# Kernel optimization log

Hardware: AMD Instinct MI355X
Metric: run time of the kernel (lower is better)

## Reference

```python
import jax, jax.numpy as jnp
import numpy as np

B, N, C, H = 256, 197, 768, 12
D = C // H  # 64
GRID = 14   # h = w = int(N**0.5); N-1 == 14*14


def setup_inputs() -> dict:
    key = jax.random.key(0)
    ks = jax.random.split(key, 5)
    s = 0.02
    return {
        "x": jax.random.normal(ks[0], (B, N, C), dtype=jnp.float32),
        "W_qkv": jax.random.normal(ks[1], (C, 3 * C), dtype=jnp.float32) * s,
        "b_qkv": jnp.zeros((3 * C,), dtype=jnp.float32),
        "W_proj": jax.random.normal(ks[2], (C, C), dtype=jnp.float32) * s,
        "b_proj": jnp.zeros((C,), dtype=jnp.float32),
        "dwc_w": jax.random.normal(ks[3], (C, 1, 3, 3), dtype=jnp.float32) * s,
        "dwc_b": jnp.zeros((C,), dtype=jnp.float32),
    }


def reference(x, W_qkv, b_qkv, W_proj, b_proj, dwc_w, dwc_b):
    Bx, Nx, Cx = x.shape
    Dh = Cx // H
    h = w = GRID
    # qkv projection -> (3, B, H, N, D)
    qkv = (x @ W_qkv + b_qkv).reshape(Bx, Nx, 3, H, Dh).transpose(2, 0, 3, 1, 4)
    q, k, v = qkv[0], qkv[1], qkv[2]
    scale = Dh ** -0.5
    # graph-candidate attention (softmax candidate): (B, H, N, N)
    attn = jax.nn.softmax(jnp.einsum('bhnd,bhmd->bhnm', q, k) * scale, axis=-1)
    out = jnp.einsum('bhnm,bhmd->bhnd', attn, v)
    out = out.transpose(0, 2, 1, 3).reshape(Bx, Nx, Cx)
    # depthwise conv on V (excluding cls token), residual add into rows 1:
    v_ = v[:, :, 1:, :].transpose(0, 2, 1, 3).reshape(Bx, h, w, Cx).transpose(0, 3, 1, 2)  # (B,C,h,w)
    conv = jax.lax.conv_general_dilated(
        v_, dwc_w, window_strides=(1, 1), padding='SAME',
        feature_group_count=Cx,
        dimension_numbers=('NCHW', 'OIHW', 'NCHW'),
    ) + dwc_b[None, :, None, None]
    out = out.at[:, 1:, :].add(conv.transpose(0, 2, 3, 1).reshape(Bx, Nx - 1, Cx))
    return out @ W_proj + b_proj
```

## Files before the change

kernel.cpp:

```cpp
#include <hip/hip_runtime.h>
#include <hip/hip_bf16.h>

typedef __attribute__((ext_vector_type(8))) short s16x8;
typedef __attribute__((ext_vector_type(4))) float f32x4;

#define MFMA(a, b, c) __builtin_amdgcn_mfma_f32_16x16x32_bf16((a), (b), (c), 0, 0, 0)

__device__ __forceinline__ short f2bf(float f) {
  unsigned u = __builtin_bit_cast(unsigned, f);
  u += 0x7FFFu + ((u >> 16) & 1u);
  return (short)(u >> 16);
}
__device__ __forceinline__ float bf2f(short s) {
  unsigned u = ((unsigned)(unsigned short)s) << 16;
  return __builtin_bit_cast(float, u);
}
__device__ __forceinline__ void async16(const void* g, void* l) {
  __builtin_amdgcn_global_load_lds((const __attribute__((address_space(1))) void*)g,
                                   (__attribute__((address_space(3))) void*)l, 16, 0, 0);
}


__global__ __launch_bounds__(256) void f32_to_bf16_k(const float* __restrict__ in,
                                                     short* __restrict__ out, int n4) {
  int i = blockIdx.x * 256 + threadIdx.x;
  if (i >= n4) return;
  float4 v = ((const float4*)in)[i];
  short4 o;
  o.x = f2bf(v.x); o.y = f2bf(v.y); o.z = f2bf(v.z); o.w = f2bf(v.w);
  ((short4*)out)[i] = o;
}

__global__ __launch_bounds__(256) void transpose_bf16_k(const float* __restrict__ in,
                                                        short* __restrict__ out, int K, int N) {
  int idx = blockIdx.x * 256 + threadIdx.x;
  if (idx >= K * N) return;
  int n = idx / K;
  int k = idx - n * K;
  out[idx] = f2bf(in[k * N + n]);
}

__global__ __launch_bounds__(256) void transpose_dwc_k(const float* __restrict__ in,
                                                       float* __restrict__ out) {
  int idx = blockIdx.x * 256 + threadIdx.x;
  if (idx >= 9 * 768) return;
  int c = idx % 768;
  int tap = idx / 768;
  out[idx] = in[c * 9 + tap];
}


__device__ __forceinline__ void gemm_core(const short* __restrict__ A, const short* __restrict__ Bt,
                                          short* Asm, short* Bsm, int m0, int n0,
                                          f32x4 (&acc)[4][4]) {
  const int tid = threadIdx.x;
  const int lane = tid & 63;
  const int w = tid >> 6;
  const int wm = w >> 1, wn = w & 1;
  const int l15 = lane & 15, qd = lane >> 4;

  for (int kt = 0; kt < 12; ++kt) {
    __syncthreads();
#pragma unroll
    for (int i = 0; i < 4; ++i) {
      int s = i * 256 + tid;
      int row = s >> 3, cst = s & 7;
      int cg = cst ^ (row & 7);
      async16(A + (m0 + row) * 768 + kt * 64 + cg * 8, Asm + s * 8);
      async16(Bt + (n0 + row) * 768 + kt * 64 + cg * 8, Bsm + s * 8);
    }
    __builtin_amdgcn_s_waitcnt(0x0f70);
    __syncthreads();
#pragma unroll
    for (int ks = 0; ks < 2; ++ks) {
      s16x8 af[4], bfr[4];
#pragma unroll
      for (int mt = 0; mt < 4; ++mt) {
        int row = wm * 64 + mt * 16 + l15;
        int kc = ks * 4 + qd;
        af[mt] = *(const s16x8*)(Asm + row * 64 + ((kc ^ (row & 7)) << 3));
      }
#pragma unroll
      for (int nt = 0; nt < 4; ++nt) {
        int row = wn * 64 + nt * 16 + l15;
        int kc = ks * 4 + qd;
        bfr[nt] = *(const s16x8*)(Bsm + row * 64 + ((kc ^ (row & 7)) << 3));
      }
#pragma unroll
      for (int mt = 0; mt < 4; ++mt)
#pragma unroll
        for (int nt = 0; nt < 4; ++nt)
          acc[mt][nt] = MFMA(af[mt], bfr[nt], acc[mt][nt]);
    }
  }
}

__device__ __forceinline__ int xcd_remap(int orig, int nwg) {
  int xcd = orig & 7;
  int grp = orig >> 3;
  int q = nwg >> 3, r = nwg & 7;
  return (xcd < r ? xcd * (q + 1) : r * (q + 1) + (xcd - r) * q) + grp;
}

__global__ __launch_bounds__(256) void gemm_qkv(const short* __restrict__ A, const short* __restrict__ Bt,
                                                const float* __restrict__ bias,
                                                short* __restrict__ qo, short* __restrict__ ko,
                                                short* __restrict__ vo) {
  __shared__ short Asm[128 * 64];
  __shared__ short Bsm[128 * 64];
  const int nwg = 394 * 18;
  int wgid = xcd_remap(blockIdx.x, nwg);
  int mt0 = wgid / 18;
  int nt0 = wgid - mt0 * 18;
  const int m0 = mt0 * 128;
  const int n0 = nt0 * 128;
  const f32x4 z4 = {0.f, 0.f, 0.f, 0.f};
  f32x4 acc[4][4];
#pragma unroll
  for (int i = 0; i < 4; ++i)
#pragma unroll
    for (int j = 0; j < 4; ++j) acc[i][j] = z4;
  gemm_core(A, Bt, Asm, Bsm, m0, n0, acc);

  const int tid = threadIdx.x, lane = tid & 63, w = tid >> 6;
  const int wm = w >> 1, wn = w & 1, l15 = lane & 15, qd = lane >> 4;

  float bv[4];
  short* dstp[4];
  int coff[4];
#pragma unroll
  for (int nt = 0; nt < 4; ++nt) {
    int n = n0 + wn * 64 + nt * 16 + l15;
    bv[nt] = bias[n];
    int s = n / 768;
    int rem = n - s * 768;
    int hh = rem >> 6, d = rem & 63;
    dstp[nt] = (s == 0) ? qo : ((s == 1) ? ko : vo);
    coff[nt] = hh * 197 * 64 + d;
  }
#pragma unroll
  for (int mt = 0; mt < 4; ++mt) {
#pragma unroll
    for (int r = 0; r < 4; ++r) {
      int m = m0 + wm * 64 + mt * 16 + qd * 4 + r;
      int bb = m / 197;
      int tok = m - bb * 197;
      size_t base = (size_t)bb * (12 * 197 * 64) + (size_t)tok * 64;
#pragma unroll
      for (int nt = 0; nt < 4; ++nt)
        dstp[nt][base + coff[nt]] = f2bf(acc[mt][nt][r] + bv[nt]);
    }
  }
}

__global__ __launch_bounds__(256) void gemm_proj(const short* __restrict__ A, const short* __restrict__ Bt,
                                                 const float* __restrict__ bias,
                                                 float* __restrict__ out) {
  __shared__ short Asm[128 * 64];
  __shared__ short Bsm[128 * 64];
  const int nwg = 394 * 6;
  int wgid = xcd_remap(blockIdx.x, nwg);
  int mt0 = wgid / 6;
  int nt0 = wgid - mt0 * 6;
  const int m0 = mt0 * 128;
  const int n0 = nt0 * 128;
  const f32x4 z4 = {0.f, 0.f, 0.f, 0.f};
  f32x4 acc[4][4];
#pragma unroll
  for (int i = 0; i < 4; ++i)
#pragma unroll
    for (int j = 0; j < 4; ++j) acc[i][j] = z4;
  gemm_core(A, Bt, Asm, Bsm, m0, n0, acc);

  const int tid = threadIdx.x, lane = tid & 63, w = tid >> 6;
  const int wm = w >> 1, wn = w & 1, l15 = lane & 15, qd = lane >> 4;
#pragma unroll
  for (int mt = 0; mt < 4; ++mt) {
#pragma unroll
    for (int r = 0; r < 4; ++r) {
      int m = m0 + wm * 64 + mt * 16 + qd * 4 + r;
      float* orow = out + (size_t)m * 768;
#pragma unroll
      for (int nt = 0; nt < 4; ++nt) {
        int n = n0 + wn * 64 + nt * 16 + l15;
        orow[n] = acc[mt][nt][r] + bias[n];
      }
    }
  }
}

__global__ __launch_bounds__(256) void attn_fused(const short* __restrict__ qa, const short* __restrict__ ka,
                                                  const short* __restrict__ va,
                                                  short* __restrict__ aout) {
  __shared__ short Klds[197 * 64];
  __shared__ short Vt[64 * 256];
  __shared__ short Plds[4][16 * 40];

  const int tid = threadIdx.x;
  const int lane = tid & 63;
  const int w = tid >> 6;
  const int l15 = lane & 15, qd = lane >> 4;
  const int bh = blockIdx.x;
  const int b = bh / 12;
  const int h = bh - b * 12;
  const short* kb = ka + (size_t)bh * (197 * 64);
  const short* vb = va + (size_t)bh * (197 * 64);
  const short* qb = qa + (size_t)bh * (197 * 64);

  for (int c = tid; c < 197 * 8; c += 256) {
    int row = c >> 3, cc = c & 7;
    s16x8 v8 = *(const s16x8*)(kb + row * 64 + cc * 8);
    *(s16x8*)(Klds + row * 64 + ((cc ^ (row & 7)) << 3)) = v8;
  }
  for (int c = tid; c < 197 * 8; c += 256) {
    int key = c >> 3, cc = c & 7;
    s16x8 v8 = *(const s16x8*)(vb + key * 64 + cc * 8);
    int kc = key >> 3, km = key & 7;
#pragma unroll
    for (int j = 0; j < 8; ++j) {
      int d = cc * 8 + j;
      Vt[d * 256 + ((kc ^ (d & 7)) << 3) + km] = v8[j];
    }
  }
  for (int i = tid; i < 64 * 27; i += 256) {
    int d = i / 27;
    int key = 197 + (i - d * 27);
    Vt[d * 256 + (((key >> 3) ^ (d & 7)) << 3) + (key & 7)] = 0;
  }
  __syncthreads();

  for (int qt = w; qt < 13; qt += 4) {
    const int m0 = qt * 16;
    int mrow = m0 + l15; if (mrow > 196) mrow = 196;
    s16x8 qf0 = *(const s16x8*)(qb + mrow * 64 + qd * 8);
    s16x8 qf1 = *(const s16x8*)(qb + mrow * 64 + 32 + qd * 8);

    f32x4 S[13];
#pragma unroll
    for (int kt = 0; kt < 13; ++kt) {
      int krow = kt * 16 + l15; if (krow > 196) krow = 196;
      s16x8 kf0 = *(const s16x8*)(Klds + krow * 64 + ((qd ^ (krow & 7)) << 3));
      s16x8 kf1 = *(const s16x8*)(Klds + krow * 64 + (((4 + qd) ^ (krow & 7)) << 3));
      f32x4 sa = {0.f, 0.f, 0.f, 0.f};
      sa = MFMA(qf0, kf0, sa);
      sa = MFMA(qf1, kf1, sa);
      S[kt] = sa;
    }
    const bool maskme = (l15 > 4);
#pragma unroll
    for (int kt = 0; kt < 13; ++kt) {
#pragma unroll
      for (int r = 0; r < 4; ++r) {
        float sv = S[kt][r] * 0.125f;
        if (kt == 12 && maskme) sv = -1e30f;
        S[kt][r] = sv;
      }
    }
    float li[4];
#pragma unroll
    for (int r = 0; r < 4; ++r) {
      float m = S[0][r];
#pragma unroll
      for (int kt = 1; kt < 13; ++kt) m = fmaxf(m, S[kt][r]);
#pragma unroll
      for (int off = 1; off < 16; off <<= 1) m = fmaxf(m, __shfl_xor(m, off));
      float l = 0.f;
#pragma unroll
      for (int kt = 0; kt < 13; ++kt) {
        float p = __builtin_amdgcn_exp2f((S[kt][r] - m) * 1.44269504f);
        S[kt][r] = p;
        l += p;
      }
#pragma unroll
      for (int off = 1; off < 16; off <<= 1) l += __shfl_xor(l, off);
      li[r] = l;
    }

    const f32x4 z4 = {0.f, 0.f, 0.f, 0.f};
    f32x4 O[4] = {z4, z4, z4, z4};
    short* Pw = &Plds[w][0];
#pragma unroll
    for (int kt2 = 0; kt2 < 7; ++kt2) {
#pragma unroll
      for (int sub = 0; sub < 2; ++sub) {
        const int ktile = kt2 * 2 + sub;
#pragma unroll
        for (int r = 0; r < 4; ++r) {
          short pv = 0;
          if (ktile < 13) pv = f2bf(S[ktile][r]);
          Pw[(qd * 4 + r) * 40 + sub * 16 + l15] = pv;
        }
      }
      __builtin_amdgcn_s_waitcnt(0xc07f);
      s16x8 pf = *(const s16x8*)(Pw + l15 * 40 + qd * 8);
#pragma unroll
      for (int nt = 0; nt < 4; ++nt) {
        int d = nt * 16 + l15;
        s16x8 vf = *(const s16x8*)(Vt + d * 256 + (((kt2 * 4 + qd) ^ (d & 7)) << 3));
        O[nt] = MFMA(pf, vf, O[nt]);
      }
    }

#pragma unroll
    for (int r = 0; r < 4; ++r) {
      int tok = m0 + qd * 4 + r;
      if (tok > 196) continue;
      float linv = __builtin_amdgcn_rcpf(li[r]);
      size_t ob = ((size_t)b * 197 + tok) * 768 + h * 64;
#pragma unroll
      for (int nt = 0; nt < 4; ++nt) {
        int d = nt * 16 + l15;
        aout[ob + d] = f2bf(O[nt][r] * linv);
      }
    }
  }
}

__global__ __launch_bounds__(256) void dwconv_add_k(const short* __restrict__ va,
                                                    const float* __restrict__ wT,
                                                    const float* __restrict__ dwcb,
                                                    short* __restrict__ aout) {
  int idx = blockIdx.x * 256 + threadIdx.x;
  if (idx >= 256 * 196 * 96) return;
  int ch = idx % 96;
  int rest = idx / 96;
  int p = rest % 196;
  int b = rest / 196;
  int y = p / 14, x = p - y * 14;
  int c0 = ch * 8;
  int h = c0 >> 6, d0 = c0 & 63;
  const short* vrow = va + (size_t)(b * 12 + h) * (197 * 64) + d0;

  float acc[8];
  float4 b0 = *(const float4*)(dwcb + c0);
  float4 b1 = *(const float4*)(dwcb + c0 + 4);
  acc[0] = b0.x; acc[1] = b0.y; acc[2] = b0.z; acc[3] = b0.w;
  acc[4] = b1.x; acc[5] = b1.y; acc[6] = b1.z; acc[7] = b1.w;

#pragma unroll
  for (int dy = -1; dy <= 1; ++dy) {
    int yy = y + dy;
    if (yy < 0 || yy > 13) continue;
#pragma unroll
    for (int dx = -1; dx <= 1; ++dx) {
      int xx = x + dx;
      if (xx < 0 || xx > 13) continue;
      int key = 1 + yy * 14 + xx;
      s16x8 v8 = *(const s16x8*)(vrow + (size_t)key * 64);
      int tap = (dy + 1) * 3 + (dx + 1);
      const float* wrow = wT + tap * 768 + c0;
      float4 w0 = *(const float4*)(wrow);
      float4 w1 = *(const float4*)(wrow + 4);
      acc[0] += w0.x * bf2f(v8[0]);
      acc[1] += w0.y * bf2f(v8[1]);
      acc[2] += w0.z * bf2f(v8[2]);
      acc[3] += w0.w * bf2f(v8[3]);
      acc[4] += w1.x * bf2f(v8[4]);
      acc[5] += w1.y * bf2f(v8[5]);
      acc[6] += w1.z * bf2f(v8[6]);
      acc[7] += w1.w * bf2f(v8[7]);
    }
  }

  size_t ao = ((size_t)b * 197 + (1 + p)) * 768 + c0;
  s16x8 a8 = *(const s16x8*)(aout + ao);
  s16x8 o8;
#pragma unroll
  for (int j = 0; j < 8; ++j) o8[j] = f2bf(bf2f(a8[j]) + acc[j]);
  *(s16x8*)(aout + ao) = o8;
}


extern "C" void kernel_launch(void* const* d_in, const int* in_sizes, int n_in,
                              void* d_out, int out_size, void* d_ws, size_t ws_size,
                              hipStream_t stream) {
  const float* x     = (const float*)d_in[0];
  const float* Wqkv  = (const float*)d_in[1];
  const float* bqkv  = (const float*)d_in[2];
  const float* Wproj = (const float*)d_in[3];
  const float* bproj = (const float*)d_in[4];
  const float* dwcw  = (const float*)d_in[5];
  const float* dwcb  = (const float*)d_in[6];
  float* out = (float*)d_out;

  const size_t XE = (size_t)50432 * 768;
  short* ws     = (short*)d_ws;
  short* xbf    = ws;
  short* wqkvT  = xbf + XE;
  short* wprojT = wqkvT + (size_t)2304 * 768;
  short* qarr   = wprojT + (size_t)768 * 768;
  short* karr   = qarr + XE;
  short* varr   = karr + XE;
  short* aoutb  = xbf;
  float* wT     = (float*)wqkvT;

  f32_to_bf16_k<<<(int)((XE / 4 + 255) / 256), 256, 0, stream>>>(x, xbf, (int)(XE / 4));
  transpose_bf16_k<<<(2304 * 768 + 255) / 256, 256, 0, stream>>>(Wqkv, wqkvT, 768, 2304);
  transpose_bf16_k<<<(768 * 768 + 255) / 256, 256, 0, stream>>>(Wproj, wprojT, 768, 768);
  gemm_qkv<<<394 * 18, 256, 0, stream>>>(xbf, wqkvT, bqkv, qarr, karr, varr);
  transpose_dwc_k<<<27, 256, 0, stream>>>(dwcw, wT);
  attn_fused<<<3072, 256, 0, stream>>>(qarr, karr, varr, aoutb);
  dwconv_add_k<<<(256 * 196 * 96) / 256, 256, 0, stream>>>(varr, wT, dwcb, aoutb);
  gemm_proj<<<394 * 6, 256, 0, stream>>>(aoutb, wprojT, bproj, out);
}
```

Before: 890.1 us.

## Use 256x256-tile GEMMs with a 4-stage async LDS pipeline

Replaces the 128x128, 256-thread GEMM core for the QKV and output projections with a 256x256, 512-thread core. The new core uses K-steps of 32 and a 4-slot ring of async global-to-LDS loads, keeping three stages in flight. Partial vmcnt waits let loads overlap the MFMA work, and s_setprio is raised around the MFMA block. This aims to increase operand reuse per tile and hide global load latency. The cost is 128KB of dynamic LDS, which limits each CU to one workgroup, and a coarser grid that makes the tail wave larger.

```diff
diff --git a/kernel.cpp b/kernel.cpp
--- a/kernel.cpp
+++ b/kernel.cpp
@@ -49,52 +49,6 @@
   out[idx] = in[c * 9 + tap];
 }
 
-
-__device__ __forceinline__ void gemm_core(const short* __restrict__ A, const short* __restrict__ Bt,
-                                          short* Asm, short* Bsm, int m0, int n0,
-                                          f32x4 (&acc)[4][4]) {
-  const int tid = threadIdx.x;
-  const int lane = tid & 63;
-  const int w = tid >> 6;
-  const int wm = w >> 1, wn = w & 1;
-  const int l15 = lane & 15, qd = lane >> 4;
-
-  for (int kt = 0; kt < 12; ++kt) {
-    __syncthreads();
-#pragma unroll
-    for (int i = 0; i < 4; ++i) {
-      int s = i * 256 + tid;
-      int row = s >> 3, cst = s & 7;
-      int cg = cst ^ (row & 7);
-      async16(A + (m0 + row) * 768 + kt * 64 + cg * 8, Asm + s * 8);
-      async16(Bt + (n0 + row) * 768 + kt * 64 + cg * 8, Bsm + s * 8);
-    }
-    __builtin_amdgcn_s_waitcnt(0x0f70);
-    __syncthreads();
-#pragma unroll
-    for (int ks = 0; ks < 2; ++ks) {
-      s16x8 af[4], bfr[4];
-#pragma unroll
-      for (int mt = 0; mt < 4; ++mt) {
-        int row = wm * 64 + mt * 16 + l15;
-        int kc = ks * 4 + qd;
-        af[mt] = *(const s16x8*)(Asm + row * 64 + ((kc ^ (row & 7)) << 3));
-      }
-#pragma unroll
-      for (int nt = 0; nt < 4; ++nt) {
-        int row = wn * 64 + nt * 16 + l15;
-        int kc = ks * 4 + qd;
-        bfr[nt] = *(const s16x8*)(Bsm + row * 64 + ((kc ^ (row & 7)) << 3));
-      }
-#pragma unroll
-      for (int mt = 0; mt < 4; ++mt)
-#pragma unroll
-        for (int nt = 0; nt < 4; ++nt)
-          acc[mt][nt] = MFMA(af[mt], bfr[nt], acc[mt][nt]);
-    }
-  }
-}
-
 __device__ __forceinline__ int xcd_remap(int orig, int nwg) {
   int xcd = orig & 7;
   int grp = orig >> 3;
@@ -102,28 +56,112 @@
   return (xcd < r ? xcd * (q + 1) : r * (q + 1) + (xcd - r) * q) + grp;
 }
 
-__global__ __launch_bounds__(256) void gemm_qkv(const short* __restrict__ A, const short* __restrict__ Bt,
-                                                const float* __restrict__ bias,
-                                                short* __restrict__ qo, short* __restrict__ ko,
-                                                short* __restrict__ vo) {
-  __shared__ short Asm[128 * 64];
-  __shared__ short Bsm[128 * 64];
-  const int nwg = 394 * 18;
+
+__device__ __forceinline__ void gemm256_core(const short* __restrict__ A,
+                                             const short* __restrict__ Bt,
+                                             short* Asm, short* Bsm,
+                                             int m0, int n0, f32x4 (&acc)[8][4]) {
+  const int tid = threadIdx.x;
+  const int lane = tid & 63;
+  const int w = tid >> 6;
+  const int wm = w >> 2, wn = w & 3;
+  const int l15 = lane & 15, qd = lane >> 4;
+  const int arow0 = wm * 128, bcol0 = wn * 64;
+
+  auto STAGE = [&](int t) {
+    const int slot = t & 3;
+    short* As = Asm + slot * 8192;
+    short* Bs = Bsm + slot * 8192;
+#pragma unroll
+    for (int j = 0; j < 2; ++j) {
+      int s = j * 512 + tid;
+      int row = s >> 2, cst = s & 3;
+      int cg = cst ^ (row & 3);
+      async16(A + (size_t)(m0 + row) * 768 + t * 32 + cg * 8, As + s * 8);
+      async16(Bt + (size_t)(n0 + row) * 768 + t * 32 + cg * 8, Bs + s * 8);
+    }
+  };
+
+  auto COMPUTE = [&](int t) {
+    const int slot = t & 3;
+    const short* As = Asm + slot * 8192;
+    const short* Bs = Bsm + slot * 8192;
+    s16x8 af[8], bfr[4];
+#pragma unroll
+    for (int mt = 0; mt < 8; ++mt) {
+      int row = arow0 + mt * 16 + l15;
+      af[mt] = *(const s16x8*)(As + row * 32 + ((qd ^ (row & 3)) << 3));
+    }
+#pragma unroll
+    for (int nt = 0; nt < 4; ++nt) {
+      int row = bcol0 + nt * 16 + l15;
+      bfr[nt] = *(const s16x8*)(Bs + row * 32 + ((qd ^ (row & 3)) << 3));
+    }
+    __builtin_amdgcn_s_setprio(1);
+#pragma unroll
+    for (int mt = 0; mt < 8; ++mt)
+#pragma unroll
+      for (int nt = 0; nt < 4; ++nt)
+        acc[mt][nt] = MFMA(af[mt], bfr[nt], acc[mt][nt]);
+    __builtin_amdgcn_s_setprio(0);
+  };
+
+  STAGE(0);
+  __builtin_amdgcn_sched_barrier(0);
+  STAGE(1);
+  __builtin_amdgcn_sched_barrier(0);
+  STAGE(2);
+  __builtin_amdgcn_sched_barrier(0);
+
+  for (int t = 0; t < 21; ++t) {
+    STAGE(t + 3);
+    __builtin_amdgcn_sched_barrier(0);
+    __builtin_amdgcn_s_waitcnt(0x0f7c);
+    __builtin_amdgcn_s_barrier();
+    __builtin_amdgcn_sched_barrier(0);
+    COMPUTE(t);
+    __builtin_amdgcn_sched_barrier(0);
+    __builtin_amdgcn_s_barrier();
+    __builtin_amdgcn_sched_barrier(0);
+  }
+  __builtin_amdgcn_s_waitcnt(0x0f78);
+  __builtin_amdgcn_s_barrier();
+  __builtin_amdgcn_sched_barrier(0);
+  COMPUTE(21);
+  __builtin_amdgcn_s_barrier();
+  __builtin_amdgcn_s_waitcnt(0x0f74);
+  __builtin_amdgcn_s_barrier();
+  __builtin_amdgcn_sched_barrier(0);
+  COMPUTE(22);
+  __builtin_amdgcn_s_barrier();
+  __builtin_amdgcn_s_waitcnt(0x0f70);
+  __builtin_amdgcn_s_barrier();
+  __builtin_amdgcn_sched_barrier(0);
+  COMPUTE(23);
+}
+
+__global__ __launch_bounds__(512, 2) void gemm_qkv256(const short* __restrict__ A,
+                                                      const short* __restrict__ Bt,
+                                                      const float* __restrict__ bias,
+                                                      short* __restrict__ qo, short* __restrict__ ko,
+                                                      short* __restrict__ vo) {
+  extern __shared__ short smem[];
+  const int nwg = 197 * 9;
   int wgid = xcd_remap(blockIdx.x, nwg);
-  int mt0 = wgid / 18;
-  int nt0 = wgid - mt0 * 18;
-  const int m0 = mt0 * 128;
-  const int n0 = nt0 * 128;
+  int mt0 = wgid / 9;
+  int nt0 = wgid - mt0 * 9;
+  const int m0 = mt0 * 256;
+  const int n0 = nt0 * 256;
   const f32x4 z4 = {0.f, 0.f, 0.f, 0.f};
-  f32x4 acc[4][4];
-#pragma unroll
-  for (int i = 0; i < 4; ++i)
+  f32x4 acc[8][4];
+#pragma unroll
+  for (int i = 0; i < 8; ++i)
 #pragma unroll
     for (int j = 0; j < 4; ++j) acc[i][j] = z4;
-  gemm_core(A, Bt, Asm, Bsm, m0, n0, acc);
+  gemm256_core(A, Bt, smem, smem + 32768, m0, n0, acc);
 
   const int tid = threadIdx.x, lane = tid & 63, w = tid >> 6;
-  const int wm = w >> 1, wn = w & 1, l15 = lane & 15, qd = lane >> 4;
+  const int wm = w >> 2, wn = w & 3, l15 = lane & 15, qd = lane >> 4;
 
   float bv[4];
   short* dstp[4];
@@ -139,10 +177,10 @@
     coff[nt] = hh * 197 * 64 + d;
   }
 #pragma unroll
-  for (int mt = 0; mt < 4; ++mt) {
+  for (int mt = 0; mt < 8; ++mt) {
 #pragma unroll
     for (int r = 0; r < 4; ++r) {
-      int m = m0 + wm * 64 + mt * 16 + qd * 4 + r;
+      int m = m0 + wm * 128 + mt * 16 + qd * 4 + r;
       int bb = m / 197;
       int tok = m - bb * 197;
       size_t base = (size_t)bb * (12 * 197 * 64) + (size_t)tok * 64;
@@ -153,32 +191,32 @@
   }
 }
 
-__global__ __launch_bounds__(256) void gemm_proj(const short* __restrict__ A, const short* __restrict__ Bt,
-                                                 const float* __restrict__ bias,
-                                                 float* __restrict__ out) {
-  __shared__ short Asm[128 * 64];
-  __shared__ short Bsm[128 * 64];
-  const int nwg = 394 * 6;
+__global__ __launch_bounds__(512, 2) void gemm_proj256(const short* __restrict__ A,
+                                                       const short* __restrict__ Bt,
+                                                       const float* __restrict__ bias,
+                                                       float* __restrict__ out) {
+  extern __shared__ short smem[];
+  const int nwg = 197 * 3;
   int wgid = xcd_remap(blockIdx.x, nwg);
-  int mt0 = wgid / 6;
-  int nt0 = wgid - mt0 * 6;
-  const int m0 = mt0 * 128;
-  const int n0 = nt0 * 128;
+  int mt0 = wgid / 3;
+  int nt0 = wgid - mt0 * 3;
+  const int m0 = mt0 * 256;
+  const int n0 = nt0 * 256;
   const f32x4 z4 = {0.f, 0.f, 0.f, 0.f};
-  f32x4 acc[4][4];
-#pragma unroll
-  for (int i = 0; i < 4; ++i)
+  f32x4 acc[8][4];
+#pragma unroll
+  for (int i = 0; i < 8; ++i)
 #pragma unroll
     for (int j = 0; j < 4; ++j) acc[i][j] = z4;
-  gemm_core(A, Bt, Asm, Bsm, m0, n0, acc);
+  gemm256_core(A, Bt, smem, smem + 32768, m0, n0, acc);
 
   const int tid = threadIdx.x, lane = tid & 63, w = tid >> 6;
-  const int wm = w >> 1, wn = w & 1, l15 = lane & 15, qd = lane >> 4;
-#pragma unroll
-  for (int mt = 0; mt < 4; ++mt) {
+  const int wm = w >> 2, wn = w & 3, l15 = lane & 15, qd = lane >> 4;
+#pragma unroll
+  for (int mt = 0; mt < 8; ++mt) {
 #pragma unroll
     for (int r = 0; r < 4; ++r) {
-      int m = m0 + wm * 64 + mt * 16 + qd * 4 + r;
+      int m = m0 + wm * 128 + mt * 16 + qd * 4 + r;
       float* orow = out + (size_t)m * 768;
 #pragma unroll
       for (int nt = 0; nt < 4; ++nt) {
@@ -202,10 +240,10 @@
   const int l15 = lane & 15, qd = lane >> 4;
   const int bh = blockIdx.x;
   const int b = bh / 12;
-  const int h = bh - b * 12;
   const short* kb = ka + (size_t)bh * (197 * 64);
   const short* vb = va + (size_t)bh * (197 * 64);
   const short* qb = qa + (size_t)bh * (197 * 64);
+  const int h = bh - b * 12;
 
   for (int c = tid; c < 197 * 8; c += 256) {
     int row = c >> 3, cc = c & 7;
@@ -394,12 +432,19 @@
   short* aoutb  = xbf;
   float* wT     = (float*)wqkvT;
 
+  static bool attr_set = false;
+  if (!attr_set) {
+    hipFuncSetAttribute((const void*)gemm_qkv256, hipFuncAttributeMaxDynamicSharedMemorySize, 131072);
+    hipFuncSetAttribute((const void*)gemm_proj256, hipFuncAttributeMaxDynamicSharedMemorySize, 131072);
+    attr_set = true;
+  }
+
   f32_to_bf16_k<<<(int)((XE / 4 + 255) / 256), 256, 0, stream>>>(x, xbf, (int)(XE / 4));
   transpose_bf16_k<<<(2304 * 768 + 255) / 256, 256, 0, stream>>>(Wqkv, wqkvT, 768, 2304);
   transpose_bf16_k<<<(768 * 768 + 255) / 256, 256, 0, stream>>>(Wproj, wprojT, 768, 768);
-  gemm_qkv<<<394 * 18, 256, 0, stream>>>(xbf, wqkvT, bqkv, qarr, karr, varr);
+  gemm_qkv256<<<197 * 9, 512, 131072, stream>>>(xbf, wqkvT, bqkv, qarr, karr, varr);
   transpose_dwc_k<<<27, 256, 0, stream>>>(dwcw, wT);
   attn_fused<<<3072, 256, 0, stream>>>(qarr, karr, varr, aoutb);
   dwconv_add_k<<<(256 * 196 * 96) / 256, 256, 0, stream>>>(varr, wT, dwcb, aoutb);
-  gemm_proj<<<394 * 6, 256, 0, stream>>>(aoutb, wprojT, bproj, out);
-}
+  gemm_proj256<<<197 * 3, 512, 131072, stream>>>(aoutb, wprojT, bproj, out);
+}
```

After: 840.0 us. -5.6%, faster.
